# Kernel tuning notes

Hardware: AMD Instinct MI355X
Metric: run time of the kernel (lower is better)

## Reference

```python
import jax, jax.numpy as jnp
import numpy as np

D_EMBED, D_K, D_V = 1024, 64, 64
B, S = 4, 4096


def setup_inputs() -> dict:
    key = jax.random.key(0)
    k1, k2, k3, k4 = jax.random.split(key, 4)
    x = jax.random.normal(k1, (B, S, D_EMBED), dtype=jnp.float32)
    # nn.Linear(d_embed, d) stores weight as [d, d_embed]
    Wq = jax.random.normal(k2, (D_K, D_EMBED), dtype=jnp.float32) * (D_EMBED ** -0.5)
    Wk = jax.random.normal(k3, (D_K, D_EMBED), dtype=jnp.float32) * (D_EMBED ** -0.5)
    Wv = jax.random.normal(k4, (D_V, D_EMBED), dtype=jnp.float32) * (D_EMBED ** -0.5)
    return {"x": x, "Wq": Wq, "Wk": Wk, "Wv": Wv}


def reference(x, Wq, Wk, Wv):
    # self-attention: y = z = x
    key = jnp.einsum('bse,ke->bsk', x, Wk)
    query = jnp.einsum('bse,ke->bsk', x, Wq)
    value = jnp.einsum('bse,ve->bsv', x, Wv)
    d_k = key.shape[-1]
    weight = jnp.einsum('bqk,bsk->bqs', query, key) / (d_k ** 0.5)
    # Faithful to torch: tril then masked_fill(weight == 0, -inf)
    weight = jnp.tril(weight)
    weight = jnp.where(weight == 0, -jnp.inf, weight)
    weight = jax.nn.softmax(weight, axis=-1)
    return jnp.einsum('bqs,bsv->bqv', weight, value)
```

## Files before the change

kernel.cpp:

```cpp
#include <hip/hip_runtime.h>
#include <hip/hip_bf16.h>


typedef short s16x8 __attribute__((ext_vector_type(8)));
typedef float f32x4 __attribute__((ext_vector_type(4)));
typedef float f32x16 __attribute__((ext_vector_type(16)));
typedef unsigned u32x2 __attribute__((ext_vector_type(2)));

#define MFMA16(a, b, c) __builtin_amdgcn_mfma_f32_16x16x32_bf16(a, b, c, 0, 0, 0)
#define MFMA32(a, b, c) __builtin_amdgcn_mfma_f32_32x32x16_bf16(a, b, c, 0, 0, 0)

constexpr int SEQ = 4096;
constexpr int DE  = 1024;

__device__ __forceinline__ short f2bf(float f) {
    union { float f; unsigned u; } v; v.f = f;
    unsigned r = (v.u + 0x7FFFu + ((v.u >> 16) & 1u)) >> 16;
    return (short)r;
}
__device__ __forceinline__ unsigned fbits(float f) { union { float f; unsigned u; } v; v.f = f; return v.u; }
__device__ __forceinline__ float bitsf(unsigned u) { union { unsigned u; float f; } v; v.u = u; return v.f; }
__device__ __forceinline__ unsigned pk2(float a, float b) {
    return (fbits(b) & 0xFFFF0000u) | (fbits(a) >> 16);
}

#define GLDS(gp, lp)                                                          \
    __builtin_amdgcn_global_load_lds(                                         \
        (const __attribute__((address_space(1))) unsigned int*)(gp),          \
        (__attribute__((address_space(3))) unsigned int*)(lp), 16, 0, 0)

__global__ __launch_bounds__(256) void k_convw(const float* __restrict__ Wq,
                                               const float* __restrict__ Wk,
                                               const float* __restrict__ Wv,
                                               short* __restrict__ Wb) {
    int i = (blockIdx.x * 256 + threadIdx.x) * 4;
    if (i >= 192 * 1024) return;
    int n = i >> 10, k = i & 1023;
    const float* src; float sc;
    if (n < 64)       { src = Wq + n * 1024;         sc = 0.18033688011112042f; }
    else if (n < 128) { src = Wk + (n - 64) * 1024;  sc = 1.0f; }
    else              { src = Wv + (n - 128) * 1024; sc = 1.0f; }
    float4 v = *(const float4*)(src + k);
    short4 o;
    o.x = f2bf(v.x * sc); o.y = f2bf(v.y * sc);
    o.z = f2bf(v.z * sc); o.w = f2bf(v.w * sc);
    *(short4*)(Wb + i) = o;
}

__global__ __launch_bounds__(512, 4) void k_proj(const float* __restrict__ x,
                                                 const short* __restrict__ Wb,
                                                 short* __restrict__ Qs,
                                                 short* __restrict__ Ks,
                                                 short* __restrict__ Vt) {
    __shared__ __align__(16) char lds[2][32768];
    const int tid  = threadIdx.x;
    const int lane = tid & 63;
    const int c = lane & 15, g = (lane >> 4) & 3;
    const int wv = tid >> 6;
    const int rg = wv & 1, nh = wv >> 1;
    const int n0 = nh * 48;
    const int m0 = blockIdx.x * 32;

    const int Ar  = tid >> 4;
    const int Acs = ((tid & 15) << 4) ^ ((Ar & 7) << 4);
    const char* aS0 = (const char*)x + (((size_t)(m0 + Ar)) << 12) + Acs;
    const int Wr  = tid >> 3;
    const int Wcs = ((tid & 7) << 4) ^ ((Wr & 7) << 4);
    const char* wS0 = (const char*)Wb + (((size_t)Wr) << 11) + Wcs;
    const char* wS1 = wS0 + ((size_t)64 << 11);
    const char* wS2 = wS0 + ((size_t)128 << 11);

    char* db0 = &lds[0][0] + tid * 16;
    char* db1 = &lds[1][0] + tid * 16;

    const int arow = rg * 16 + c;
    const int swz  = (c & 7) << 4;
    const char* aR[2] = { &lds[0][0] + arow * 256, &lds[1][0] + arow * 256 };
    const char* wR[2][3];
#pragma unroll
    for (int nf = 0; nf < 3; nf++) {
        int wrow = n0 + nf * 16 + c;
        wR[0][nf] = &lds[0][0] + 8192 + wrow * 128;
        wR[1][nf] = &lds[1][0] + 8192 + wrow * 128;
    }

    f32x4 acc[3];
#pragma unroll
    for (int i = 0; i < 3; i++) acc[i] = (f32x4){0.f, 0.f, 0.f, 0.f};

#define PSTAGE(kk, db) {                                  \
        GLDS(aS0 + (kk) * 256, (db));                     \
        GLDS(wS0 + (kk) * 128, (db) + 8192);              \
        GLDS(wS1 + (kk) * 128, (db) + 16384);             \
        GLDS(wS2 + (kk) * 128, (db) + 24576); }

#define PCOMPUTE(bi) {                                                         \
        _Pragma("unroll")                                                      \
        for (int kc = 0; kc < 2; kc++) {                                       \
            float4 a0 = *(const float4*)(aR[bi] + ((kc*128 + g*32)      ^ swz)); \
            float4 a1 = *(const float4*)(aR[bi] + ((kc*128 + g*32 + 16) ^ swz)); \
            s16x8 a;                                                           \
            a[0]=f2bf(a0.x); a[1]=f2bf(a0.y); a[2]=f2bf(a0.z); a[3]=f2bf(a0.w); \
            a[4]=f2bf(a1.x); a[5]=f2bf(a1.y); a[6]=f2bf(a1.z); a[7]=f2bf(a1.w); \
            _Pragma("unroll")                                                  \
            for (int nf = 0; nf < 3; nf++) {                                   \
                s16x8 bfr = *(const s16x8*)(wR[bi][nf] + ((kc*64 + g*16) ^ swz)); \
                acc[nf] = MFMA16(a, bfr, acc[nf]);                             \
            }                                                                  \
        } }

    PSTAGE(0, db0);
    PSTAGE(1, db1);

    for (int kk = 0; kk < 15; kk++) {
        asm volatile("s_waitcnt vmcnt(4)" ::: "memory");
        __builtin_amdgcn_sched_barrier(0);
        __builtin_amdgcn_s_barrier();
        if (kk & 1) PCOMPUTE(1) else PCOMPUTE(0)
        asm volatile("s_waitcnt lgkmcnt(0)" ::: "memory");
        __builtin_amdgcn_sched_barrier(0);
        __builtin_amdgcn_s_barrier();
        if (kk < 14) { if (kk & 1) PSTAGE(kk + 2, db1) else PSTAGE(kk + 2, db0) }
    }
    asm volatile("s_waitcnt vmcnt(0)" ::: "memory");
    __builtin_amdgcn_sched_barrier(0);
    __builtin_amdgcn_s_barrier();
    PCOMPUTE(1)
#undef PSTAGE
#undef PCOMPUTE

#pragma unroll
    for (int nf = 0; nf < 3; nf++) {
        int col16 = n0 + nf * 16;
        if (col16 < 64) {
            int col = col16 + c;
#pragma unroll
            for (int r = 0; r < 4; r++)
                Qs[(size_t)(m0 + rg * 16 + g * 4 + r) * 64 + col] = f2bf(acc[nf][r]);
        } else if (col16 < 128) {
            int col = col16 - 64 + c;
#pragma unroll
            for (int r = 0; r < 4; r++)
                Ks[(size_t)(m0 + rg * 16 + g * 4 + r) * 64 + col] = f2bf(acc[nf][r]);
        } else {
            int d  = col16 - 128 + c;
            int mm = m0 + rg * 16 + g * 4;
            int bt = mm >> 12, s0 = mm & (SEQ - 1);
            short4 o;
            o.x = f2bf(acc[nf][0]); o.y = f2bf(acc[nf][1]);
            o.z = f2bf(acc[nf][2]); o.w = f2bf(acc[nf][3]);
            *(short4*)(Vt + ((size_t)(bt * 64 + d)) * SEQ + s0) = o;
        }
    }
}

__global__ __launch_bounds__(256, 2) void k_attn(const short* __restrict__ Qs,
                                                 const short* __restrict__ Ks,
                                                 const short* __restrict__ Vt,
                                                 float* __restrict__ pws) {
    __shared__ __align__(16) char smem[65536];
    float (*pO)[64][33] = (float (*)[64][33])smem;
    float* pM = (float*)(smem + 33792);
    float* pL = pM + 128;

    int tid = threadIdx.x;
    int l = tid & 63, wv = tid >> 6;
    int q = l & 31, hi = l >> 5;

    int ub = blockIdx.x >> 2, bt = blockIdx.x & 3;
    int j, seg;
    if (ub < 128)      { j = 127 - (ub >> 2);       seg = ub & 3; }
    else if (ub < 224) { int t = ub - 128; j = 95 - t / 3;  seg = t - (t / 3) * 3; }
    else if (ub < 288) { int t = ub - 224; j = 63 - (t >> 1); seg = t & 1; }
    else               { j = 31 - (ub - 288);       seg = 0; }

    int q0 = j * 32;
    int kbase = seg << 10;
    int kend_u = min(q0 + 32, kbase + 1024);
    const int R = (kend_u - kbase + 127) >> 7;

    const short* Qb = Qs + (size_t)bt * SEQ * 64;
    const short* Kb = Ks + (size_t)bt * SEQ * 64;
    const short* Vb = Vt + (size_t)bt * 64 * SEQ;

    s16x8 qf[4];
#pragma unroll
    for (int d = 0; d < 4; d++)
        qf[d] = *(const s16x8*)(Qb + (size_t)(q0 + q) * 64 + d * 16 + hi * 8);

    const int kr  = l >> 3;
    const int kch = (l & 7) ^ kr;
    const int vr  = l >> 4;

#define ASTAGE(kb2, bufb) {                                                    \
        _Pragma("unroll")                                                      \
        for (int i = 0; i < 4; i++)                                            \
            GLDS(Kb + (((size_t)((kb2) + wv*32 + i*8 + kr)) << 6) + kch*8,     \
                 smem + (bufb)*32768 + (wv*4 + i)*1024);                       \
        _Pragma("unroll")                                                      \
        for (int i = 0; i < 4; i++)                                            \
            GLDS(Vb + (size_t)(wv*16 + i*4 + vr) * SEQ + (kb2)                 \
                    + (((l & 15) ^ (i*4 + vr)) * 8),                           \
                 smem + (bufb)*32768 + 16384 + (wv*4 + i)*1024); }

    f32x16 o0 = {}, o1 = {};
    float m = -1e30f, ll = 0.f;

    ASTAGE(kbase, 0);
    ASTAGE(kbase + 128, 1);

    for (int r = 0; r < R; r++) {
        if (r == R - 1) asm volatile("s_waitcnt vmcnt(0)" ::: "memory");
        else            asm volatile("s_waitcnt vmcnt(8)" ::: "memory");
        __builtin_amdgcn_sched_barrier(0);
        __builtin_amdgcn_s_barrier();
        __builtin_amdgcn_sched_barrier(0);

        int k0 = kbase + r * 128 + wv * 32;
        if (k0 < kend_u) {
            const char* kb = smem + (r & 1) * 32768 + (wv * 32 + q) * 128;
            int ks = q & 7;
            s16x8 ka0 = *(const s16x8*)(kb + (((hi    ) ^ ks) << 4));
            s16x8 ka1 = *(const s16x8*)(kb + (((hi + 2) ^ ks) << 4));
            s16x8 ka2 = *(const s16x8*)(kb + (((hi + 4) ^ ks) << 4));
            s16x8 ka3 = *(const s16x8*)(kb + (((hi + 6) ^ ks) << 4));
            f32x16 s = {};
            s = MFMA32(ka0, qf[0], s);
            s = MFMA32(ka1, qf[1], s);
            s = MFMA32(ka2, qf[2], s);
            s = MFMA32(ka3, qf[3], s);

            if (k0 + 31 > q0) {
#pragma unroll
                for (int rr = 0; rr < 16; rr++) {
                    int kk = k0 + (rr & 3) + 8 * (rr >> 2) + 4 * hi;
                    if (kk > q0 + q) s[rr] = -3.0e38f;
                }
            }

            float t0 = fmaxf(fmaxf(fmaxf(s[0], s[1]), fmaxf(s[2], s[3])),
                             fmaxf(fmaxf(s[4], s[5]), fmaxf(s[6], s[7])));
            float t1 = fmaxf(fmaxf(fmaxf(s[8], s[9]), fmaxf(s[10], s[11])),
                             fmaxf(fmaxf(s[12], s[13]), fmaxf(s[14], s[15])));
            float tm = fmaxf(t0, t1);
            u32x2 sw = __builtin_amdgcn_permlane32_swap(fbits(tm), fbits(tm), false, false);
            tm = fmaxf(bitsf(sw[0]), bitsf(sw[1]));
            float mn = fmaxf(m, tm);
            float scale = __builtin_amdgcn_exp2f(m - mn);
            m = mn;
#pragma unroll
            for (int rr = 0; rr < 16; rr++) s[rr] = __builtin_amdgcn_exp2f(s[rr] - mn);
            float u0s = ((s[0] + s[1]) + (s[2] + s[3])) + ((s[4] + s[5]) + (s[6] + s[7]));
            float u1s = ((s[8] + s[9]) + (s[10] + s[11])) + ((s[12] + s[13]) + (s[14] + s[15]));
            float ts = u0s + u1s;
            sw = __builtin_amdgcn_permlane32_swap(fbits(ts), fbits(ts), false, false);
            ts = bitsf(sw[0]) + bitsf(sw[1]);
            ll = ll * scale + ts;
            o0 *= scale; o1 *= scale;

            unsigned A0 = pk2(s[0], s[1]),   B0 = pk2(s[2], s[3]);
            unsigned A1 = pk2(s[4], s[5]),   B1 = pk2(s[6], s[7]);
            unsigned A2 = pk2(s[8], s[9]),   B2 = pk2(s[10], s[11]);
            unsigned A3 = pk2(s[12], s[13]), B3 = pk2(s[14], s[15]);
            u32x2 r0 = __builtin_amdgcn_permlane32_swap(A0, A1, false, false);
            u32x2 r1 = __builtin_amdgcn_permlane32_swap(B0, B1, false, false);
            u32x2 r2 = __builtin_amdgcn_permlane32_swap(A2, A3, false, false);
            u32x2 r3 = __builtin_amdgcn_permlane32_swap(B2, B3, false, false);
            union { unsigned u[4]; s16x8 v; } p0u, p1u;
            p0u.u[0] = r0[0]; p0u.u[1] = r1[0]; p0u.u[2] = r0[1]; p0u.u[3] = r1[1];
            p1u.u[0] = r2[0]; p1u.u[1] = r3[0]; p1u.u[2] = r2[1]; p1u.u[3] = r3[1];

            const char* vbb = smem + (r & 1) * 32768 + 16384;
            int vc0 = ((4 * wv + hi)     ^ (q & 15)) << 4;
            int vc1 = ((4 * wv + hi + 2) ^ (q & 15)) << 4;
            const char* v0p = vbb + q * 256;
            const char* v1p = vbb + (q + 32) * 256;
            o0 = MFMA32(*(const s16x8*)(v0p + vc0), p0u.v, o0);
            o0 = MFMA32(*(const s16x8*)(v0p + vc1), p1u.v, o0);
            o1 = MFMA32(*(const s16x8*)(v1p + vc0), p0u.v, o1);
            o1 = MFMA32(*(const s16x8*)(v1p + vc1), p1u.v, o1);
        }

        asm volatile("s_waitcnt lgkmcnt(0)" ::: "memory");
        __builtin_amdgcn_sched_barrier(0);
        __builtin_amdgcn_s_barrier();
        if (r + 2 < R) { if (r & 1) ASTAGE(kbase + (r + 2) * 128, 1) else ASTAGE(kbase + (r + 2) * 128, 0) }
    }
#undef ASTAGE

#pragma unroll
    for (int rr = 0; rr < 16; rr++) {
        int dv = (rr & 3) + 8 * (rr >> 2) + 4 * hi;
        pO[wv][dv][q]      = o0[rr];
        pO[wv][dv + 32][q] = o1[rr];
    }
    if (hi == 0) { pM[wv * 32 + q] = m; pL[wv * 32 + q] = ll; }
    __syncthreads();

    int q2 = tid >> 3, d0 = (tid & 7) * 8;
    float m0v = pM[q2], m1v = pM[32 + q2], m2v = pM[64 + q2], m3v = pM[96 + q2];
    float M = fmaxf(fmaxf(m0v, m1v), fmaxf(m2v, m3v));
    float w0 = __builtin_amdgcn_exp2f(m0v - M);
    float w1 = __builtin_amdgcn_exp2f(m1v - M);
    float w2 = __builtin_amdgcn_exp2f(m2v - M);
    float w3 = __builtin_amdgcn_exp2f(m3v - M);
    float L = w0 * pL[q2] + w1 * pL[32 + q2] + w2 * pL[64 + q2] + w3 * pL[96 + q2];
    float res[8];
#pragma unroll
    for (int i = 0; i < 8; i++)
        res[i] = w0 * pO[0][d0 + i][q2] + w1 * pO[1][d0 + i][q2]
               + w2 * pO[2][d0 + i][q2] + w3 * pO[3][d0 + i][q2];
    float* p = pws + (size_t)(((bt << 7) + j) * 4 + seg) * 2112;
    float4 f0 = {res[0], res[1], res[2], res[3]};
    float4 f1 = {res[4], res[5], res[6], res[7]};
    *(float4*)(p + q2 * 64 + d0) = f0;
    *(float4*)(p + q2 * 64 + d0 + 4) = f1;
    if ((tid & 7) == 0) { p[2048 + q2] = M; p[2080 + q2] = L; }
}

__global__ __launch_bounds__(256) void k_comb(const float* __restrict__ pws,
                                              float* __restrict__ out) {
    int bid = blockIdx.x;
    int bt = bid >> 7, j = bid & 127;
    int nseg = (j >> 5) + 1;
    int tid = threadIdx.x;
    int q2 = tid >> 3, d0 = (tid & 7) * 8;
    const float* base = pws + (size_t)(bid * 4) * 2112;

    float ms[4], wsg[4];
    float M = -1e30f;
#pragma unroll 4
    for (int s = 0; s < nseg; s++) { ms[s] = base[s * 2112 + 2048 + q2]; M = fmaxf(M, ms[s]); }
    float L = 0.f;
#pragma unroll 4
    for (int s = 0; s < nseg; s++) {
        wsg[s] = __builtin_amdgcn_exp2f(ms[s] - M);
        L += wsg[s] * base[s * 2112 + 2080 + q2];
    }
    float inv = 1.0f / L;
    float res[8];
#pragma unroll
    for (int i = 0; i < 8; i++) res[i] = 0.f;
#pragma unroll 4
    for (int s = 0; s < nseg; s++) {
        const float* po = base + s * 2112 + q2 * 64 + d0;
#pragma unroll
        for (int i = 0; i < 8; i++) res[i] += wsg[s] * po[i];
    }
    float* op = out + ((size_t)bt * SEQ + j * 32 + q2) * 64 + d0;
    float4 f0 = {res[0] * inv, res[1] * inv, res[2] * inv, res[3] * inv};
    float4 f1 = {res[4] * inv, res[5] * inv, res[6] * inv, res[7] * inv};
    *(float4*)op = f0;
    *(float4*)(op + 4) = f1;
}

extern "C" void kernel_launch(void* const* d_in, const int* in_sizes, int n_in,
                              void* d_out, int out_size, void* d_ws, size_t ws_size,
                              hipStream_t stream) {
    const float* x  = (const float*)d_in[0];
    const float* Wq = (const float*)d_in[1];
    const float* Wk = (const float*)d_in[2];
    const float* Wv = (const float*)d_in[3];
    float* out = (float*)d_out;

    char* ws = (char*)d_ws;
    short* Wb = (short*)ws;
    short* Qs = (short*)(ws + 393216);
    short* Ks = (short*)(ws + 393216 + 2097152);
    short* Vt = (short*)(ws + 393216 + 2 * 2097152);
    float* pP = (float*)(ws + 6684672);

    k_convw<<<dim3(192),  dim3(256), 0, stream>>>(Wq, Wk, Wv, Wb);
    k_proj <<<dim3(512),  dim3(512), 0, stream>>>(x, Wb, Qs, Ks, Vt);
    k_attn <<<dim3(1280), dim3(256), 0, stream>>>(Qs, Ks, Vt, pP);
    k_comb <<<dim3(512),  dim3(256), 0, stream>>>(pP, out);
}
```

Measured before the change: 63.10 us.

## Retile projection to read weights from global, add lazy softmax rescale and MFMA priority

The projection kernel now handles 64 rows per block with 6 accumulator fragments per wave. Weight fragments are loaded straight from global memory (cache) instead of being staged through LDS, so LDS holds only the x tile and the grid is halved. The attention kernel skips the running-max rescale unless some lane's max grows by more than 8 (in log2 units), which saves exp and multiply work at some numerical risk. It also raises wave priority around the MFMA blocks and adds a barrier before reusing shared memory in the epilogue.

```diff
diff --git a/kernel.cpp b/kernel.cpp
--- a/kernel.cpp
+++ b/kernel.cpp
@@ -47,28 +47,24 @@
     *(short4*)(Wb + i) = o;
 }
 
-__global__ __launch_bounds__(512, 4) void k_proj(const float* __restrict__ x,
-                                                 const short* __restrict__ Wb,
-                                                 short* __restrict__ Qs,
-                                                 short* __restrict__ Ks,
-                                                 short* __restrict__ Vt) {
-    __shared__ __align__(16) char lds[2][32768];
+__global__ __launch_bounds__(512) void k_proj(const float* __restrict__ x,
+                                              const short* __restrict__ Wb,
+                                              short* __restrict__ Qs,
+                                              short* __restrict__ Ks,
+                                              short* __restrict__ Vt) {
+    __shared__ __align__(16) char lds[2][16384];
     const int tid  = threadIdx.x;
     const int lane = tid & 63;
     const int c = lane & 15, g = (lane >> 4) & 3;
     const int wv = tid >> 6;
-    const int rg = wv & 1, nh = wv >> 1;
-    const int n0 = nh * 48;
-    const int m0 = blockIdx.x * 32;
+    const int rg = wv & 3, nh = wv >> 2;
+    const int n0 = nh * 96;
+    const int m0 = blockIdx.x * 64;
 
     const int Ar  = tid >> 4;
     const int Acs = ((tid & 15) << 4) ^ ((Ar & 7) << 4);
     const char* aS0 = (const char*)x + (((size_t)(m0 + Ar)) << 12) + Acs;
-    const int Wr  = tid >> 3;
-    const int Wcs = ((tid & 7) << 4) ^ ((Wr & 7) << 4);
-    const char* wS0 = (const char*)Wb + (((size_t)Wr) << 11) + Wcs;
-    const char* wS1 = wS0 + ((size_t)64 << 11);
-    const char* wS2 = wS0 + ((size_t)128 << 11);
+    const char* aS1 = aS0 + ((size_t)32 << 12);
 
     char* db0 = &lds[0][0] + tid * 16;
     char* db1 = &lds[1][0] + tid * 16;
@@ -76,25 +72,15 @@
     const int arow = rg * 16 + c;
     const int swz  = (c & 7) << 4;
     const char* aR[2] = { &lds[0][0] + arow * 256, &lds[1][0] + arow * 256 };
-    const char* wR[2][3];
-#pragma unroll
-    for (int nf = 0; nf < 3; nf++) {
-        int wrow = n0 + nf * 16 + c;
-        wR[0][nf] = &lds[0][0] + 8192 + wrow * 128;
-        wR[1][nf] = &lds[1][0] + 8192 + wrow * 128;
-    }
-
-    f32x4 acc[3];
-#pragma unroll
-    for (int i = 0; i < 3; i++) acc[i] = (f32x4){0.f, 0.f, 0.f, 0.f};
-
-#define PSTAGE(kk, db) {                                  \
-        GLDS(aS0 + (kk) * 256, (db));                     \
-        GLDS(wS0 + (kk) * 128, (db) + 8192);              \
-        GLDS(wS1 + (kk) * 128, (db) + 16384);             \
-        GLDS(wS2 + (kk) * 128, (db) + 24576); }
-
-#define PCOMPUTE(bi) {                                                         \
+    const short* wb0 = Wb + (size_t)(n0 + c) * DE + g * 8;
+
+    f32x4 acc[6];
+#pragma unroll
+    for (int i = 0; i < 6; i++) acc[i] = (f32x4){0.f, 0.f, 0.f, 0.f};
+
+#define PSTAGE(kk, db) { GLDS(aS0 + (kk) * 256, (db)); GLDS(aS1 + (kk) * 256, (db) + 8192); }
+
+#define PCOMPUTE(bi, kk) {                                                     \
         _Pragma("unroll")                                                      \
         for (int kc = 0; kc < 2; kc++) {                                       \
             float4 a0 = *(const float4*)(aR[bi] + ((kc*128 + g*32)      ^ swz)); \
@@ -103,8 +89,8 @@
             a[0]=f2bf(a0.x); a[1]=f2bf(a0.y); a[2]=f2bf(a0.z); a[3]=f2bf(a0.w); \
             a[4]=f2bf(a1.x); a[5]=f2bf(a1.y); a[6]=f2bf(a1.z); a[7]=f2bf(a1.w); \
             _Pragma("unroll")                                                  \
-            for (int nf = 0; nf < 3; nf++) {                                   \
-                s16x8 bfr = *(const s16x8*)(wR[bi][nf] + ((kc*64 + g*16) ^ swz)); \
+            for (int nf = 0; nf < 6; nf++) {                                   \
+                s16x8 bfr = *(const s16x8*)(wb0 + (size_t)nf * 16 * DE + (kk) * 64 + kc * 32); \
                 acc[nf] = MFMA16(a, bfr, acc[nf]);                             \
             }                                                                  \
         } }
@@ -112,25 +98,22 @@
     PSTAGE(0, db0);
     PSTAGE(1, db1);
 
-    for (int kk = 0; kk < 15; kk++) {
-        asm volatile("s_waitcnt vmcnt(4)" ::: "memory");
+    for (int kk = 0; kk < 16; kk++) {
+        if (kk == 15) asm volatile("s_waitcnt vmcnt(0)" ::: "memory");
+        else          asm volatile("s_waitcnt vmcnt(2)" ::: "memory");
         __builtin_amdgcn_sched_barrier(0);
         __builtin_amdgcn_s_barrier();
-        if (kk & 1) PCOMPUTE(1) else PCOMPUTE(0)
+        if (kk & 1) PCOMPUTE(1, kk) else PCOMPUTE(0, kk)
         asm volatile("s_waitcnt lgkmcnt(0)" ::: "memory");
         __builtin_amdgcn_sched_barrier(0);
         __builtin_amdgcn_s_barrier();
         if (kk < 14) { if (kk & 1) PSTAGE(kk + 2, db1) else PSTAGE(kk + 2, db0) }
     }
-    asm volatile("s_waitcnt vmcnt(0)" ::: "memory");
-    __builtin_amdgcn_sched_barrier(0);
-    __builtin_amdgcn_s_barrier();
-    PCOMPUTE(1)
 #undef PSTAGE
 #undef PCOMPUTE
 
 #pragma unroll
-    for (int nf = 0; nf < 3; nf++) {
+    for (int nf = 0; nf < 6; nf++) {
         int col16 = n0 + nf * 16;
         if (col16 < 64) {
             int col = col16 + c;
@@ -225,10 +208,12 @@
             s16x8 ka2 = *(const s16x8*)(kb + (((hi + 4) ^ ks) << 4));
             s16x8 ka3 = *(const s16x8*)(kb + (((hi + 6) ^ ks) << 4));
             f32x16 s = {};
+            __builtin_amdgcn_s_setprio(1);
             s = MFMA32(ka0, qf[0], s);
             s = MFMA32(ka1, qf[1], s);
             s = MFMA32(ka2, qf[2], s);
             s = MFMA32(ka3, qf[3], s);
+            __builtin_amdgcn_s_setprio(0);
 
             if (k0 + 31 > q0) {
 #pragma unroll
@@ -245,18 +230,21 @@
             float tm = fmaxf(t0, t1);
             u32x2 sw = __builtin_amdgcn_permlane32_swap(fbits(tm), fbits(tm), false, false);
             tm = fmaxf(bitsf(sw[0]), bitsf(sw[1]));
-            float mn = fmaxf(m, tm);
-            float scale = __builtin_amdgcn_exp2f(m - mn);
-            m = mn;
-#pragma unroll
-            for (int rr = 0; rr < 16; rr++) s[rr] = __builtin_amdgcn_exp2f(s[rr] - mn);
+            if (__any(tm > m + 8.0f)) {
+                float mn = fmaxf(m, tm);
+                float scale = __builtin_amdgcn_exp2f(m - mn);
+                m = mn;
+                ll *= scale;
+                o0 *= scale; o1 *= scale;
+            }
+#pragma unroll
+            for (int rr = 0; rr < 16; rr++) s[rr] = __builtin_amdgcn_exp2f(s[rr] - m);
             float u0s = ((s[0] + s[1]) + (s[2] + s[3])) + ((s[4] + s[5]) + (s[6] + s[7]));
             float u1s = ((s[8] + s[9]) + (s[10] + s[11])) + ((s[12] + s[13]) + (s[14] + s[15]));
             float ts = u0s + u1s;
             sw = __builtin_amdgcn_permlane32_swap(fbits(ts), fbits(ts), false, false);
             ts = bitsf(sw[0]) + bitsf(sw[1]);
-            ll = ll * scale + ts;
-            o0 *= scale; o1 *= scale;
+            ll += ts;
 
             unsigned A0 = pk2(s[0], s[1]),   B0 = pk2(s[2], s[3]);
             unsigned A1 = pk2(s[4], s[5]),   B1 = pk2(s[6], s[7]);
@@ -275,10 +263,12 @@
             int vc1 = ((4 * wv + hi + 2) ^ (q & 15)) << 4;
             const char* v0p = vbb + q * 256;
             const char* v1p = vbb + (q + 32) * 256;
+            __builtin_amdgcn_s_setprio(1);
             o0 = MFMA32(*(const s16x8*)(v0p + vc0), p0u.v, o0);
             o0 = MFMA32(*(const s16x8*)(v0p + vc1), p1u.v, o0);
             o1 = MFMA32(*(const s16x8*)(v1p + vc0), p0u.v, o1);
             o1 = MFMA32(*(const s16x8*)(v1p + vc1), p1u.v, o1);
+            __builtin_amdgcn_s_setprio(0);
         }
 
         asm volatile("s_waitcnt lgkmcnt(0)" ::: "memory");
@@ -288,6 +278,7 @@
     }
 #undef ASTAGE
 
+    __syncthreads();
 #pragma unroll
     for (int rr = 0; rr < 16; rr++) {
         int dv = (rr & 3) + 8 * (rr >> 2) + 4 * hi;
@@ -371,7 +362,7 @@
     float* pP = (float*)(ws + 6684672);
 
     k_convw<<<dim3(192),  dim3(256), 0, stream>>>(Wq, Wk, Wv, Wb);
-    k_proj <<<dim3(512),  dim3(512), 0, stream>>>(x, Wb, Qs, Ks, Vt);
+    k_proj <<<dim3(256),  dim3(512), 0, stream>>>(x, Wb, Qs, Ks, Vt);
     k_attn <<<dim3(1280), dim3(256), 0, stream>>>(Qs, Ks, Vt, pP);
     k_comb <<<dim3(512),  dim3(256), 0, stream>>>(pP, out);
 }
```

New measurement: 103.1 us. +63.3%, slower.
